# Optimization experiments

Measured on AMD Instinct MI355X. Metric: run time of the kernel, lower is better.

## Reference

```python
import jax, jax.numpy as jnp
import numpy as np

B_SZ, N_INST, D_IN, D_OUT, C_COMP, M_RANK = 512, 4, 1024, 1024, 64, 256

def setup_inputs() -> dict:
    key = jax.random.key(0)
    k1, k2, k3, k4 = jax.random.split(key, 4)
    x = jax.random.normal(k1, (B_SZ, N_INST, D_IN), dtype=jnp.float32)
    A = jax.random.normal(k2, (N_INST, C_COMP, D_IN, M_RANK), dtype=jnp.float32) * 0.02
    Bp = jax.random.normal(k3, (N_INST, C_COMP, M_RANK, D_OUT), dtype=jnp.float32) * 0.02
    topk_mask = jax.random.randint(k4, (B_SZ, N_INST, C_COMP), 0, 2, dtype=jnp.int32)
    return {"x": x, "A": A, "B": Bp, "topk_mask": topk_mask}

def reference(x, A, B, topk_mask):
    # inner: [b, i, C, m]
    inner = jnp.einsum('bid,icdm->bicm', x, A)
    inner = inner * topk_mask.astype(inner.dtype)[..., None]
    # comp: [b, i, C, d_out]
    comp = jnp.einsum('bicm,icmo->bico', inner, B)
    # sum over components C -> [b, i, d_out]
    return comp.sum(axis=2)
```

## Files before the change

kernel.cpp:

```cpp
#include <hip/hip_runtime.h>
#include <hip/hip_bf16.h>
#include <stdint.h>

#define B_SZ   512
#define NINST  4
#define D_IN   1024
#define D_OUTD 1024
#define CCOMP  64
#define MRANK  256
#define KTOT   (CCOMP*MRANK)

typedef __attribute__((ext_vector_type(4))) float  f32x4;
typedef __attribute__((ext_vector_type(8))) __bf16 bf16x8;
typedef __attribute__((ext_vector_type(4))) __bf16 bf16x4;

__device__ inline void gload_lds16(const __bf16* g, __bf16* l) {
  __builtin_amdgcn_global_load_lds(
      (const __attribute__((address_space(1))) void*)g,
      (__attribute__((address_space(3))) void*)l, 16, 0, 0);
}

__global__ __launch_bounds__(256)
void xcvt_kernel(const float* __restrict__ x, __bf16* __restrict__ xbf)
{
  const int total = (B_SZ*NINST*D_IN) / 4;
  for (int v = blockIdx.x*256 + threadIdx.x; v < total; v += gridDim.x*256) {
    const int k4 = v & 255;
    const int i  = (v >> 8) & 3;
    const int b  = v >> 10;
    f32x4 f = ((const f32x4*)x)[v];
    bf16x4 h; h[0]=(__bf16)f.x; h[1]=(__bf16)f.y; h[2]=(__bf16)f.z; h[3]=(__bf16)f.w;
    ((bf16x4*)xbf)[((size_t)i*B_SZ + b)*256 + k4] = h;
  }
}

__global__ __launch_bounds__(256, 2)
void p1_kernel(const __bf16* __restrict__ xbf, const float* __restrict__ A,
               const int* __restrict__ mask, __bf16* __restrict__ inner)
{
  const int bid = blockIdx.x;
  const int L   = (bid & 7) * 64 + (bid >> 3);
  const int bt  = L & 3;
  const int mt  = (L >> 2) & 1;
  const int icg = L >> 3;
  const int ic0 = icg * 4;
  const int i   = ic0 >> 6;
  const int c0  = ic0 & 63;
  const int b0  = bt * 128;
  const int m0  = mt * 128;

  const int tid  = threadIdx.x;
  const int lane = tid & 63;
  const int wid  = tid >> 6;
  const int wr   = wid >> 1;
  const int wc   = wid & 1;

  __shared__ __align__(16) char smem[65536];
  __bf16* Xs = (__bf16*)smem;
  __bf16* As = (__bf16*)(smem + 32768);

  f32x4 acc[4][4];
#pragma unroll
  for (int a_ = 0; a_ < 4; ++a_)
#pragma unroll
    for (int b_ = 0; b_ < 4; ++b_)
      acc[a_][b_] = (f32x4){0.f, 0.f, 0.f, 0.f};

  const __bf16* xbase  = xbf + ((size_t)i * B_SZ + b0) * D_IN;
  const float*  Abase0 = A + (size_t)ic0 * D_IN * MRANK + m0;

  const int bo = tid & 127;
  const int bg = tid >> 7;

  float areg[4][8];

  auto stageXs = [&](int buf, int kt) {
#pragma unroll
    for (int q = 0; q < 4; ++q) {
      const int ci  = wid*4 + q;
      const int row = ci*8 + (lane >> 3);
      const int kch = (lane & 7) ^ (row & 7);
      gload_lds16(xbase + (size_t)row * D_IN + (kt & 15)*64 + kch*8,
                  Xs + buf*8192 + ci*512);
    }
  };
  auto loadA = [&](int kt) {
    const float* Ab = Abase0 + (size_t)(kt >> 4) * D_IN * MRANK;
#pragma unroll
    for (int q = 0; q < 4; ++q)
#pragma unroll
      for (int j = 0; j < 8; ++j)
        areg[q][j] = Ab[(size_t)((kt & 15)*64 + (bg*4+q)*8 + j)*MRANK + bo];
  };
  auto writeA = [&](int buf) {
#pragma unroll
    for (int q = 0; q < 4; ++q) {
      const int oct = bg*4 + q;
      bf16x8 h;
#pragma unroll
      for (int j = 0; j < 8; ++j) h[j] = (__bf16)areg[q][j];
      *(bf16x8*)(As + buf*8192 + bo*64 + ((oct ^ (bo & 7)))*8) = h;
    }
  };

  stageXs(0, 0); loadA(0); writeA(0);
  __syncthreads();

  int cur = 0;
  for (int kt = 0; kt < 64; ++kt) {
    if (kt+1 < 64) { stageXs(cur ^ 1, kt+1); loadA(kt+1); }
#pragma unroll
    for (int kk = 0; kk < 2; ++kk) {
      const int oct = kk*4 + (lane >> 4);
      bf16x8 af[4];
#pragma unroll
      for (int mi = 0; mi < 4; ++mi) {
        const int row = wr*64 + mi*16 + (lane & 15);
        af[mi] = *(const bf16x8*)(Xs + cur*8192 + row*64 + ((oct ^ (row & 7)))*8);
      }
#pragma unroll
      for (int ni = 0; ni < 4; ++ni) {
        const int col = wc*64 + ni*16 + (lane & 15);
        bf16x8 bfr = *(const bf16x8*)(As + cur*8192 + col*64 + ((oct ^ (col & 7)))*8);
#pragma unroll
        for (int mi = 0; mi < 4; ++mi)
          acc[mi][ni] = __builtin_amdgcn_mfma_f32_16x16x32_bf16(af[mi], bfr, acc[mi][ni], 0, 0, 0);
      }
    }
    if ((kt & 15) == 15) {
      const int c = c0 + (kt >> 4);
      __bf16* obase = inner + ((size_t)i * B_SZ + b0) * KTOT + (size_t)c * MRANK + m0;
      float mv[16];
#pragma unroll
      for (int mi = 0; mi < 4; ++mi)
#pragma unroll
        for (int j = 0; j < 4; ++j) {
          const int row = wr*64 + mi*16 + (lane >> 4)*4 + j;
          mv[mi*4+j] = (float)mask[(size_t)(b0 + row) * (NINST*CCOMP) + i*CCOMP + c];
        }
#pragma unroll
      for (int mi = 0; mi < 4; ++mi)
#pragma unroll
        for (int ni = 0; ni < 4; ++ni) {
          const int colL = wc*64 + ni*16 + (lane & 15);
#pragma unroll
          for (int j = 0; j < 4; ++j) {
            const int rowL = wr*64 + mi*16 + (lane >> 4)*4 + j;
            obase[(size_t)rowL * KTOT + colL] = (__bf16)(acc[mi][ni][j] * mv[mi*4+j]);
          }
#pragma unroll
          for (int j = 0; j < 4; ++j) acc[mi][ni][j] = 0.f;
        }
    }
    if (kt+1 < 64) writeA(cur ^ 1);
    __syncthreads();
    cur ^= 1;
  }
}

__global__ __launch_bounds__(256, 2)
void p2_kernel(const __bf16* __restrict__ inner, const float* __restrict__ Bm,
               float* __restrict__ dst, int nks)
{
  const int bid = blockIdx.x;
  const int L   = (bid & 7) * (gridDim.x >> 3) + (bid >> 3);
  const int bt  = L & 3;
  const int nt  = (L >> 2) & 7;
  const int rest = L >> 5;
  const int ks  = rest % nks;
  const int i   = rest / nks;
  const int b0  = bt * 128;
  const int o0  = nt * 128;
  const int NSTEP = (KTOT/64) / nks;
  const int kb0   = ks * NSTEP;

  const int tid  = threadIdx.x;
  const int lane = tid & 63;
  const int wid  = tid >> 6;
  const int wr   = wid >> 1;
  const int wc   = wid & 1;

  __shared__ __align__(16) char smem[65536];
  __bf16* Is = (__bf16*)smem;
  __bf16* Bs = (__bf16*)(smem + 32768);

  f32x4 acc[4][4];
#pragma unroll
  for (int a_ = 0; a_ < 4; ++a_)
#pragma unroll
    for (int b_ = 0; b_ < 4; ++b_)
      acc[a_][b_] = (f32x4){0.f, 0.f, 0.f, 0.f};

  const __bf16* ibase = inner + ((size_t)i * B_SZ + b0) * KTOT;
  const float*  Bbase = Bm + (size_t)i * KTOT * D_OUTD + o0;

  const int bo = tid & 127;
  const int bg = tid >> 7;

  float breg[4][8];

  auto stageIs = [&](int buf, int kt) {
#pragma unroll
    for (int q = 0; q < 4; ++q) {
      const int ci  = wid*4 + q;
      const int row = ci*8 + (lane >> 3);
      const int kch = (lane & 7) ^ (row & 7);
      gload_lds16(ibase + (size_t)row * KTOT + kt*64 + kch*8,
                  Is + buf*8192 + ci*512);
    }
  };
  auto loadB = [&](int kt) {
#pragma unroll
    for (int q = 0; q < 4; ++q)
#pragma unroll
      for (int j = 0; j < 8; ++j)
        breg[q][j] = Bbase[(size_t)(kt*64 + (bg*4+q)*8 + j)*D_OUTD + bo];
  };
  auto writeB = [&](int buf) {
#pragma unroll
    for (int q = 0; q < 4; ++q) {
      const int oct = bg*4 + q;
      bf16x8 h;
#pragma unroll
      for (int j = 0; j < 8; ++j) h[j] = (__bf16)breg[q][j];
      *(bf16x8*)(Bs + buf*8192 + bo*64 + ((oct ^ (bo & 7)))*8) = h;
    }
  };

  stageIs(0, kb0); loadB(kb0); writeB(0);
  __syncthreads();

  int cur = 0;
  for (int t = 0; t < NSTEP; ++t) {
    if (t+1 < NSTEP) { stageIs(cur ^ 1, kb0 + t + 1); loadB(kb0 + t + 1); }
#pragma unroll
    for (int kk = 0; kk < 2; ++kk) {
      const int oct = kk*4 + (lane >> 4);
      bf16x8 af[4];
#pragma unroll
      for (int mi = 0; mi < 4; ++mi) {
        const int row = wr*64 + mi*16 + (lane & 15);
        af[mi] = *(const bf16x8*)(Is + cur*8192 + row*64 + ((oct ^ (row & 7)))*8);
      }
#pragma unroll
      for (int ni = 0; ni < 4; ++ni) {
        const int col = wc*64 + ni*16 + (lane & 15);
        bf16x8 bfr = *(const bf16x8*)(Bs + cur*8192 + col*64 + ((oct ^ (col & 7)))*8);
#pragma unroll
        for (int mi = 0; mi < 4; ++mi)
          acc[mi][ni] = __builtin_amdgcn_mfma_f32_16x16x32_bf16(af[mi], bfr, acc[mi][ni], 0, 0, 0);
      }
    }
    if (t+1 < NSTEP) writeB(cur ^ 1);
    __syncthreads();
    cur ^= 1;
  }

  float* obase = dst + (size_t)ks * ((size_t)B_SZ*NINST*D_OUTD)
               + ((size_t)b0 * NINST + i) * D_OUTD + o0;
#pragma unroll
  for (int mi = 0; mi < 4; ++mi)
#pragma unroll
    for (int ni = 0; ni < 4; ++ni) {
      const int colL = wc*64 + ni*16 + (lane & 15);
#pragma unroll
      for (int j = 0; j < 4; ++j) {
        const int rowL = wr*64 + mi*16 + (lane >> 4)*4 + j;
        obase[(size_t)rowL * (NINST*D_OUTD) + colL] = acc[mi][ni][j];
      }
    }
}

__global__ __launch_bounds__(256)
void reduce_kernel(const float* __restrict__ part, float* __restrict__ out, int nks)
{
  const int total = (B_SZ*NINST*D_OUTD) / 4;
  for (int v = blockIdx.x*256 + threadIdx.x; v < total; v += gridDim.x*256) {
    f32x4 s = ((const f32x4*)part)[v];
    for (int ks = 1; ks < nks; ++ks)
      s += ((const f32x4*)part)[(size_t)ks*total + v];
    ((f32x4*)out)[v] = s;
  }
}

extern "C" void kernel_launch(void* const* d_in, const int* in_sizes, int n_in,
                              void* d_out, int out_size, void* d_ws, size_t ws_size,
                              hipStream_t stream) {
  const float* x    = (const float*)d_in[0];
  const float* A    = (const float*)d_in[1];
  const float* Bm   = (const float*)d_in[2];
  const int*   mask = (const int*)d_in[3];

  const size_t innerB = (size_t)NINST * B_SZ * KTOT * 2;
  const size_t xbfB   = (size_t)NINST * B_SZ * D_IN * 2;
  const size_t partB  = (size_t)B_SZ * NINST * D_OUTD * 4;

  char* p = (char*)d_ws;
  __bf16* inner = (__bf16*)p;             p += innerB;
  __bf16* xbf   = (__bf16*)p;             p += xbfB;
  const size_t used = (size_t)(p - (char*)d_ws);

  int nks = 1;
  if      (ws_size >= used + 4*partB) nks = 4;
  else if (ws_size >= used + 2*partB) nks = 2;
  float* part = (nks > 1) ? (float*)p : (float*)d_out;

  xcvt_kernel<<<dim3(1024),  dim3(256), 0, stream>>>(x, xbf);
  p1_kernel<<<dim3(512),     dim3(256), 0, stream>>>(xbf, A, mask, inner);
  p2_kernel<<<dim3(128*nks), dim3(256), 0, stream>>>(inner, Bm, part, nks);
  if (nks > 1)
    reduce_kernel<<<dim3(512), dim3(256), 0, stream>>>(part, (float*)d_out, nks);
}
```

Before: 269.2 us.

## Prefetch fp32 weight tiles two steps ahead with partial vmcnt barriers

Both GEMM kernels now keep two register sets for the fp32 A/B weight tiles and issue global loads two k-steps ahead. The main loop is unrolled by two so the register buffers alternate. The plain __syncthreads is replaced by a custom barrier that waits only until vmcnt drops to 32, so the newest prefetch stays in flight across the barrier. The goal is to hide global-load latency behind MFMA work, at the cost of more registers (which may spill or lower occupancy). The hand-tuned vmcnt counts must match the real number of outstanding loads, or LDS data could be read before it arrives.

New measurement: 1.039 ms. 3.86x slower.

```diff
diff --git a/kernel.cpp b/kernel.cpp
--- a/kernel.cpp
+++ b/kernel.cpp
@@ -19,6 +19,17 @@
       (const __attribute__((address_space(1))) void*)g,
       (__attribute__((address_space(3))) void*)l, 16, 0, 0);
 }
+
+#define BAR32() do { \
+  asm volatile("s_waitcnt lgkmcnt(0) vmcnt(32)" ::: "memory"); \
+  __builtin_amdgcn_sched_barrier(0); \
+  __builtin_amdgcn_s_barrier(); \
+  __builtin_amdgcn_sched_barrier(0); } while (0)
+#define BAR0() do { \
+  asm volatile("s_waitcnt lgkmcnt(0) vmcnt(0)" ::: "memory"); \
+  __builtin_amdgcn_sched_barrier(0); \
+  __builtin_amdgcn_s_barrier(); \
+  __builtin_amdgcn_sched_barrier(0); } while (0)
 
 __global__ __launch_bounds__(256)
 void xcvt_kernel(const float* __restrict__ x, __bf16* __restrict__ xbf)
@@ -72,7 +83,7 @@
   const int bo = tid & 127;
   const int bg = tid >> 7;
 
-  float areg[4][8];
+  float a0[4][8], a1[4][8];
 
   auto stageXs = [&](int buf, int kt) {
 #pragma unroll
@@ -84,7 +95,7 @@
                   Xs + buf*8192 + ci*512);
     }
   };
-  auto loadA = [&](int kt) {
+  auto loadA = [&](int kt, float (&areg)[4][8]) {
     const float* Ab = Abase0 + (size_t)(kt >> 4) * D_IN * MRANK;
 #pragma unroll
     for (int q = 0; q < 4; ++q)
@@ -92,7 +103,7 @@
       for (int j = 0; j < 8; ++j)
         areg[q][j] = Ab[(size_t)((kt & 15)*64 + (bg*4+q)*8 + j)*MRANK + bo];
   };
-  auto writeA = [&](int buf) {
+  auto writeA = [&](int buf, const float (&areg)[4][8]) {
 #pragma unroll
     for (int q = 0; q < 4; ++q) {
       const int oct = bg*4 + q;
@@ -102,13 +113,7 @@
       *(bf16x8*)(As + buf*8192 + bo*64 + ((oct ^ (bo & 7)))*8) = h;
     }
   };
-
-  stageXs(0, 0); loadA(0); writeA(0);
-  __syncthreads();
-
-  int cur = 0;
-  for (int kt = 0; kt < 64; ++kt) {
-    if (kt+1 < 64) { stageXs(cur ^ 1, kt+1); loadA(kt+1); }
+  auto computeStep = [&](int cur) {
 #pragma unroll
     for (int kk = 0; kk < 2; ++kk) {
       const int oct = kk*4 + (lane >> 4);
@@ -127,34 +132,56 @@
           acc[mi][ni] = __builtin_amdgcn_mfma_f32_16x16x32_bf16(af[mi], bfr, acc[mi][ni], 0, 0, 0);
       }
     }
-    if ((kt & 15) == 15) {
-      const int c = c0 + (kt >> 4);
-      __bf16* obase = inner + ((size_t)i * B_SZ + b0) * KTOT + (size_t)c * MRANK + m0;
-      float mv[16];
-#pragma unroll
-      for (int mi = 0; mi < 4; ++mi)
+  };
+  auto segEpilogue = [&](int kt) {
+    const int c = c0 + (kt >> 4);
+    __bf16* obase = inner + ((size_t)i * B_SZ + b0) * KTOT + (size_t)c * MRANK + m0;
+    float mv[16];
+#pragma unroll
+    for (int mi = 0; mi < 4; ++mi)
+#pragma unroll
+      for (int j = 0; j < 4; ++j) {
+        const int row = wr*64 + mi*16 + (lane >> 4)*4 + j;
+        mv[mi*4+j] = (float)mask[(size_t)(b0 + row) * (NINST*CCOMP) + i*CCOMP + c];
+      }
+#pragma unroll
+    for (int mi = 0; mi < 4; ++mi)
+#pragma unroll
+      for (int ni = 0; ni < 4; ++ni) {
+        const int colL = wc*64 + ni*16 + (lane & 15);
 #pragma unroll
         for (int j = 0; j < 4; ++j) {
-          const int row = wr*64 + mi*16 + (lane >> 4)*4 + j;
-          mv[mi*4+j] = (float)mask[(size_t)(b0 + row) * (NINST*CCOMP) + i*CCOMP + c];
+          const int rowL = wr*64 + mi*16 + (lane >> 4)*4 + j;
+          obase[(size_t)rowL * KTOT + colL] = (__bf16)(acc[mi][ni][j] * mv[mi*4+j]);
         }
 #pragma unroll
-      for (int mi = 0; mi < 4; ++mi)
-#pragma unroll
-        for (int ni = 0; ni < 4; ++ni) {
-          const int colL = wc*64 + ni*16 + (lane & 15);
-#pragma unroll
-          for (int j = 0; j < 4; ++j) {
-            const int rowL = wr*64 + mi*16 + (lane >> 4)*4 + j;
-            obase[(size_t)rowL * KTOT + colL] = (__bf16)(acc[mi][ni][j] * mv[mi*4+j]);
-          }
-#pragma unroll
-          for (int j = 0; j < 4; ++j) acc[mi][ni][j] = 0.f;
-        }
-    }
-    if (kt+1 < 64) writeA(cur ^ 1);
-    __syncthreads();
+        for (int j = 0; j < 4; ++j) acc[mi][ni][j] = 0.f;
+      }
+  };
+
+  stageXs(0, 0);
+  loadA(0, a0); loadA(1, a1);
+  writeA(0, a0);
+  BAR32();
+
+  int cur = 0;
+  for (int t = 0; t < 64; t += 2) {
+    if (t+1 < 64) stageXs(cur ^ 1, t+1);
+    if (t+2 < 64) loadA(t+2, a0);
+    computeStep(cur);
+    if (t+1 < 64) writeA(cur ^ 1, a1);
+    if (t < 62) BAR32(); else BAR0();
     cur ^= 1;
+    {
+      const int u = t + 1;
+      if (u+1 < 64) stageXs(cur ^ 1, u+1);
+      if (u+2 < 64) loadA(u+2, a1);
+      computeStep(cur);
+      if ((u & 15) == 15) segEpilogue(u);
+      if (u+1 < 64) writeA(cur ^ 1, a0);
+      if (u < 62) BAR32(); else BAR0();
+      cur ^= 1;
+    }
   }
 }
 
@@ -197,7 +224,7 @@
   const int bo = tid & 127;
   const int bg = tid >> 7;
 
-  float breg[4][8];
+  float b0r[4][8], b1r[4][8];
 
   auto stageIs = [&](int buf, int kt) {
 #pragma unroll
@@ -209,14 +236,14 @@
                   Is + buf*8192 + ci*512);
     }
   };
-  auto loadB = [&](int kt) {
+  auto loadB = [&](int kt, float (&breg)[4][8]) {
 #pragma unroll
     for (int q = 0; q < 4; ++q)
 #pragma unroll
       for (int j = 0; j < 8; ++j)
         breg[q][j] = Bbase[(size_t)(kt*64 + (bg*4+q)*8 + j)*D_OUTD + bo];
   };
-  auto writeB = [&](int buf) {
+  auto writeB = [&](int buf, const float (&breg)[4][8]) {
 #pragma unroll
     for (int q = 0; q < 4; ++q) {
       const int oct = bg*4 + q;
@@ -226,13 +253,7 @@
       *(bf16x8*)(Bs + buf*8192 + bo*64 + ((oct ^ (bo & 7)))*8) = h;
     }
   };
-
-  stageIs(0, kb0); loadB(kb0); writeB(0);
-  __syncthreads();
-
-  int cur = 0;
-  for (int t = 0; t < NSTEP; ++t) {
-    if (t+1 < NSTEP) { stageIs(cur ^ 1, kb0 + t + 1); loadB(kb0 + t + 1); }
+  auto computeStep = [&](int cur) {
 #pragma unroll
     for (int kk = 0; kk < 2; ++kk) {
       const int oct = kk*4 + (lane >> 4);
@@ -251,9 +272,32 @@
           acc[mi][ni] = __builtin_amdgcn_mfma_f32_16x16x32_bf16(af[mi], bfr, acc[mi][ni], 0, 0, 0);
       }
     }
-    if (t+1 < NSTEP) writeB(cur ^ 1);
-    __syncthreads();
+  };
+
+  stageIs(0, kb0);
+  loadB(kb0, b0r);
+  if (1 < NSTEP) loadB(kb0 + 1, b1r);
+  writeB(0, b0r);
+  BAR32();
+
+  int cur = 0;
+  for (int t = 0; t < NSTEP; t += 2) {
+    if (t+1 < NSTEP) stageIs(cur ^ 1, kb0 + t + 1);
+    if (t+2 < NSTEP) loadB(kb0 + t + 2, b0r);
+    computeStep(cur);
+    if (t+1 < NSTEP) writeB(cur ^ 1, b1r);
+    if (t < NSTEP-2) BAR32(); else BAR0();
     cur ^= 1;
+    {
+      const int u = t + 1;
+      if (u >= NSTEP) break;
+      if (u+1 < NSTEP) stageIs(cur ^ 1, kb0 + u + 1);
+      if (u+2 < NSTEP) loadB(kb0 + u + 2, b1r);
+      computeStep(cur);
+      if (u+1 < NSTEP) writeB(cur ^ 1, b0r);
+      if (u < NSTEP-2) BAR32(); else BAR0();
+      cur ^= 1;
+    }
   }
 
   float* obase = dst + (size_t)ks * ((size_t)B_SZ*NINST*D_OUTD)
```

## Retile p1 to 512-thread blocks with 256-row batch tiles and 32-wide K steps

Applied to the files above, without the earlier changes.

The first-stage GEMM kernel now runs 512 threads (8 waves) per block, each block covering 256 batch rows and 2 components instead of 128 rows and 4 components. The K step per stage shrinks from 64 to 32, which halves the LDS A-tile and shortens the per-thread A register staging. The aim is for each fp32 A slice that is loaded and converted to feed twice as many batch rows, cutting redundant A traffic and raising occupancy per block. In exchange each block needs twice as many barrier-separated iterations per component, and the 32-wide tiles bring a new LDS swizzle.

New measurement: 298.2 us. 10.8% more time.

```diff
diff --git a/kernel.cpp b/kernel.cpp
--- a/kernel.cpp
+++ b/kernel.cpp
@@ -34,19 +34,19 @@
   }
 }
 
-__global__ __launch_bounds__(256, 2)
+__global__ __launch_bounds__(512, 2)
 void p1_kernel(const __bf16* __restrict__ xbf, const float* __restrict__ A,
                const int* __restrict__ mask, __bf16* __restrict__ inner)
 {
   const int bid = blockIdx.x;
   const int L   = (bid & 7) * 64 + (bid >> 3);
-  const int bt  = L & 3;
-  const int mt  = (L >> 2) & 1;
-  const int icg = L >> 3;
-  const int ic0 = icg * 4;
+  const int bt  = L & 1;
+  const int mt  = (L >> 1) & 1;
+  const int icg = L >> 2;
+  const int ic0 = icg * 2;
   const int i   = ic0 >> 6;
   const int c0  = ic0 & 63;
-  const int b0  = bt * 128;
+  const int b0  = bt * 256;
   const int m0  = mt * 128;
 
   const int tid  = threadIdx.x;
@@ -55,7 +55,7 @@
   const int wr   = wid >> 1;
   const int wc   = wid & 1;
 
-  __shared__ __align__(16) char smem[65536];
+  __shared__ __align__(16) char smem[49152];
   __bf16* Xs = (__bf16*)smem;
   __bf16* As = (__bf16*)(smem + 32768);
 
@@ -66,41 +66,76 @@
     for (int b_ = 0; b_ < 4; ++b_)
       acc[a_][b_] = (f32x4){0.f, 0.f, 0.f, 0.f};
 
-  const __bf16* xbase  = xbf + ((size_t)i * B_SZ + b0) * D_IN;
-  const float*  Abase0 = A + (size_t)ic0 * D_IN * MRANK + m0;
-
-  const int bo = tid & 127;
-  const int bg = tid >> 7;
-
-  float areg[4][8];
+  const __bf16* xbase = xbf + ((size_t)i * B_SZ + b0) * D_IN;
+
+  const int am = tid & 127;
+  const int ag = tid >> 7;
+
+  float areg[8];
 
   auto stageXs = [&](int buf, int kt) {
 #pragma unroll
-    for (int q = 0; q < 4; ++q) {
-      const int ci  = wid*4 + q;
-      const int row = ci*8 + (lane >> 3);
-      const int kch = (lane & 7) ^ (row & 7);
-      gload_lds16(xbase + (size_t)row * D_IN + (kt & 15)*64 + kch*8,
+    for (int q = 0; q < 2; ++q) {
+      const int ci  = wid*2 + q;
+      const int row = ci*16 + (lane >> 2);
+      const int kch = (lane & 3) ^ (row & 3);
+      gload_lds16(xbase + (size_t)row * D_IN + (kt & 31)*32 + kch*8,
                   Xs + buf*8192 + ci*512);
     }
   };
   auto loadA = [&](int kt) {
-    const float* Ab = Abase0 + (size_t)(kt >> 4) * D_IN * MRANK;
-#pragma unroll
-    for (int q = 0; q < 4; ++q)
-#pragma unroll
-      for (int j = 0; j < 8; ++j)
-        areg[q][j] = Ab[(size_t)((kt & 15)*64 + (bg*4+q)*8 + j)*MRANK + bo];
+    const float* Ab = A + (size_t)(ic0 + (kt >> 5)) * D_IN * MRANK + m0;
+#pragma unroll
+    for (int j = 0; j < 8; ++j)
+      areg[j] = Ab[(size_t)((kt & 31)*32 + ag*8 + j)*MRANK + am];
   };
   auto writeA = [&](int buf) {
-#pragma unroll
-    for (int q = 0; q < 4; ++q) {
-      const int oct = bg*4 + q;
-      bf16x8 h;
-#pragma unroll
-      for (int j = 0; j < 8; ++j) h[j] = (__bf16)areg[q][j];
-      *(bf16x8*)(As + buf*8192 + bo*64 + ((oct ^ (bo & 7)))*8) = h;
-    }
+    bf16x8 h;
+#pragma unroll
+    for (int j = 0; j < 8; ++j) h[j] = (__bf16)areg[j];
+    *(bf16x8*)(As + buf*4096 + am*32 + ((ag ^ (am & 3)))*8) = h;
+  };
+  auto computeStep = [&](int cur) {
+    const int oct = lane >> 4;
+    bf16x8 af[4];
+#pragma unroll
+    for (int mi = 0; mi < 4; ++mi) {
+      const int row = wr*64 + mi*16 + (lane & 15);
+      af[mi] = *(const bf16x8*)(Xs + cur*8192 + row*32 + ((oct ^ (row & 3)))*8);
+    }
+#pragma unroll
+    for (int ni = 0; ni < 4; ++ni) {
+      const int col = wc*64 + ni*16 + (lane & 15);
+      bf16x8 bfr = *(const bf16x8*)(As + cur*4096 + col*32 + ((oct ^ (col & 3)))*8);
+#pragma unroll
+      for (int mi = 0; mi < 4; ++mi)
+        acc[mi][ni] = __builtin_amdgcn_mfma_f32_16x16x32_bf16(af[mi], bfr, acc[mi][ni], 0, 0, 0);
+    }
+  };
+  auto segEpilogue = [&](int kt) {
+    const int c = c0 + (kt >> 5);
+    __bf16* obase = inner + ((size_t)i * B_SZ + b0) * KTOT + (size_t)c * MRANK + m0;
+    float mv[16];
+#pragma unroll
+    for (int mi = 0; mi < 4; ++mi)
+#pragma unroll
+      for (int j = 0; j < 4; ++j) {
+        const int row = wr*64 + mi*16 + (lane >> 4)*4 + j;
+        mv[mi*4+j] = (float)mask[(size_t)(b0 + row) * (NINST*CCOMP) + i*CCOMP + c];
+      }
+#pragma unroll
+    for (int mi = 0; mi < 4; ++mi)
+#pragma unroll
+      for (int ni = 0; ni < 4; ++ni) {
+        const int colL = wc*64 + ni*16 + (lane & 15);
+#pragma unroll
+        for (int j = 0; j < 4; ++j) {
+          const int rowL = wr*64 + mi*16 + (lane >> 4)*4 + j;
+          obase[(size_t)rowL * KTOT + colL] = (__bf16)(acc[mi][ni][j] * mv[mi*4+j]);
+        }
+#pragma unroll
+        for (int j = 0; j < 4; ++j) acc[mi][ni][j] = 0.f;
+      }
   };
 
   stageXs(0, 0); loadA(0); writeA(0);
@@ -109,49 +144,8 @@
   int cur = 0;
   for (int kt = 0; kt < 64; ++kt) {
     if (kt+1 < 64) { stageXs(cur ^ 1, kt+1); loadA(kt+1); }
-#pragma unroll
-    for (int kk = 0; kk < 2; ++kk) {
-      const int oct = kk*4 + (lane >> 4);
-      bf16x8 af[4];
-#pragma unroll
-      for (int mi = 0; mi < 4; ++mi) {
-        const int row = wr*64 + mi*16 + (lane & 15);
-        af[mi] = *(const bf16x8*)(Xs + cur*8192 + row*64 + ((oct ^ (row & 7)))*8);
-      }
-#pragma unroll
-      for (int ni = 0; ni < 4; ++ni) {
-        const int col = wc*64 + ni*16 + (lane & 15);
-        bf16x8 bfr = *(const bf16x8*)(As + cur*8192 + col*64 + ((oct ^ (col & 7)))*8);
-#pragma unroll
-        for (int mi = 0; mi < 4; ++mi)
-          acc[mi][ni] = __builtin_amdgcn_mfma_f32_16x16x32_bf16(af[mi], bfr, acc[mi][ni], 0, 0, 0);
-      }
-    }
-    if ((kt & 15) == 15) {
-      const int c = c0 + (kt >> 4);
-      __bf16* obase = inner + ((size_t)i * B_SZ + b0) * KTOT + (size_t)c * MRANK + m0;
-      float mv[16];
-#pragma unroll
-      for (int mi = 0; mi < 4; ++mi)
-#pragma unroll
-        for (int j = 0; j < 4; ++j) {
-          const int row = wr*64 + mi*16 + (lane >> 4)*4 + j;
-          mv[mi*4+j] = (float)mask[(size_t)(b0 + row) * (NINST*CCOMP) + i*CCOMP + c];
-        }
-#pragma unroll
-      for (int mi = 0; mi < 4; ++mi)
-#pragma unroll
-        for (int ni = 0; ni < 4; ++ni) {
-          const int colL = wc*64 + ni*16 + (lane & 15);
-#pragma unroll
-          for (int j = 0; j < 4; ++j) {
-            const int rowL = wr*64 + mi*16 + (lane >> 4)*4 + j;
-            obase[(size_t)rowL * KTOT + colL] = (__bf16)(acc[mi][ni][j] * mv[mi*4+j]);
-          }
-#pragma unroll
-          for (int j = 0; j < 4; ++j) acc[mi][ni][j] = 0.f;
-        }
-    }
+    computeStep(cur);
+    if ((kt & 31) == 31) segEpilogue(kt);
     if (kt+1 < 64) writeA(cur ^ 1);
     __syncthreads();
     cur ^= 1;
@@ -306,7 +300,7 @@
   float* part = (nks > 1) ? (float*)p : (float*)d_out;
 
   xcvt_kernel<<<dim3(1024),  dim3(256), 0, stream>>>(x, xbf);
-  p1_kernel<<<dim3(512),     dim3(256), 0, stream>>>(xbf, A, mask, inner);
+  p1_kernel<<<dim3(512),     dim3(512), 0, stream>>>(xbf, A, mask, inner);
   p2_kernel<<<dim3(128*nks), dim3(256), 0, stream>>>(inner, Bm, part, nks);
   if (nks > 1)
     reduce_kernel<<<dim3(512), dim3(256), 0, stream>>>(part, (float*)d_out, nks);
```

## Pre-convert A to transposed bf16 and stream both GEMM operands via LDS loads

Applied to the files above, without the earlier changes.

Adds a kernel that converts A from fp32 to bf16 and transposes it so the reduction dimension is contiguous. A new first-stage GEMM then stages both x and A tiles straight into shared memory with the async global-to-LDS path, replacing per-thread fp32 register loads and conversion. The aim is to cut register pressure and conversion work in the main loop. The trade-off is extra HBM traffic on every call: a 128MB bf16 write and read-back on top of the full fp32 read of A. The new path runs only when the workspace is large enough, and it reuses the bf16 A buffer for the split-K partial sums.

New measurement: 298.4 us. 10.9% more time.

```diff
diff --git a/kernel.cpp b/kernel.cpp
--- a/kernel.cpp
+++ b/kernel.cpp
@@ -34,9 +34,159 @@
   }
 }
 
+__global__ __launch_bounds__(256)
+void atr_kernel(const float* __restrict__ A, __bf16* __restrict__ Abf)
+{
+  const int bid = blockIdx.x;
+  const int ic  = bid >> 2;
+  const int s4  = bid & 3;
+  const int i   = ic >> 6;
+  const int c   = ic & 63;
+  const int tid = threadIdx.x;
+
+  __shared__ __bf16 T[64][260];
+
+  for (int sub = 0; sub < 4; ++sub) {
+    const int d0 = s4*256 + sub*64;
+#pragma unroll
+    for (int it = 0; it < 16; ++it) {
+      const int idx = it*256 + tid;
+      const int d   = idx >> 6;
+      const int m4  = idx & 63;
+      f32x4 v = *(const f32x4*)(A + ((size_t)ic*D_IN + d0 + d)*MRANK + m4*4);
+      bf16x4 h; h[0]=(__bf16)v.x; h[1]=(__bf16)v.y; h[2]=(__bf16)v.z; h[3]=(__bf16)v.w;
+      *(bf16x4*)(&T[d][m4*4]) = h;
+    }
+    __syncthreads();
+#pragma unroll
+    for (int it = 0; it < 8; ++it) {
+      const int m   = it*32 + (tid >> 3);
+      const int dgu = tid & 7;
+      bf16x8 h;
+#pragma unroll
+      for (int j = 0; j < 8; ++j) h[j] = T[dgu*8 + j][m];
+      *(bf16x8*)(Abf + ((size_t)i*KTOT + (size_t)c*MRANK + m)*D_IN + d0 + dgu*8) = h;
+    }
+    __syncthreads();
+  }
+}
+
 __global__ __launch_bounds__(256, 2)
-void p1_kernel(const __bf16* __restrict__ xbf, const float* __restrict__ A,
-               const int* __restrict__ mask, __bf16* __restrict__ inner)
+void p1_lite(const __bf16* __restrict__ xbf, const __bf16* __restrict__ Abf,
+             const int* __restrict__ mask, __bf16* __restrict__ inner)
+{
+  const int bid = blockIdx.x;
+  const int L   = (bid & 7) * 64 + (bid >> 3);
+  const int bt  = L & 3;
+  const int ntg = (L >> 2) & 31;
+  const int i   = L >> 7;
+  const int b0  = bt * 128;
+  const int n0g = ntg * 512;
+
+  const int tid  = threadIdx.x;
+  const int lane = tid & 63;
+  const int wid  = tid >> 6;
+  const int wr   = wid >> 1;
+  const int wc   = wid & 1;
+
+  __shared__ __align__(16) char smem[65536];
+  __bf16* Xs = (__bf16*)smem;
+  __bf16* As = (__bf16*)(smem + 32768);
+
+  f32x4 acc[4][4];
+#pragma unroll
+  for (int a_ = 0; a_ < 4; ++a_)
+#pragma unroll
+    for (int b_ = 0; b_ < 4; ++b_)
+      acc[a_][b_] = (f32x4){0.f, 0.f, 0.f, 0.f};
+
+  const __bf16* xbase = xbf + ((size_t)i * B_SZ + b0) * D_IN;
+  const __bf16* abase = Abf + ((size_t)i * KTOT + n0g) * D_IN;
+
+  auto stageXs = [&](int buf, int kt) {
+#pragma unroll
+    for (int q = 0; q < 4; ++q) {
+      const int ci  = wid*4 + q;
+      const int row = ci*8 + (lane >> 3);
+      const int kch = (lane & 7) ^ (row & 7);
+      gload_lds16(xbase + (size_t)row * D_IN + (kt & 15)*64 + kch*8,
+                  Xs + buf*8192 + ci*512);
+    }
+  };
+  auto stageAs = [&](int buf, int kt) {
+    const __bf16* ab = abase + (size_t)(kt >> 4) * 128 * D_IN;
+#pragma unroll
+    for (int q = 0; q < 4; ++q) {
+      const int ci  = wid*4 + q;
+      const int row = ci*8 + (lane >> 3);
+      const int kch = (lane & 7) ^ (row & 7);
+      gload_lds16(ab + (size_t)row * D_IN + (kt & 15)*64 + kch*8,
+                  As + buf*8192 + ci*512);
+    }
+  };
+  auto computeStep = [&](int cur) {
+#pragma unroll
+    for (int kk = 0; kk < 2; ++kk) {
+      const int oct = kk*4 + (lane >> 4);
+      bf16x8 af[4];
+#pragma unroll
+      for (int mi = 0; mi < 4; ++mi) {
+        const int row = wr*64 + mi*16 + (lane & 15);
+        af[mi] = *(const bf16x8*)(Xs + cur*8192 + row*64 + ((oct ^ (row & 7)))*8);
+      }
+#pragma unroll
+      for (int ni = 0; ni < 4; ++ni) {
+        const int col = wc*64 + ni*16 + (lane & 15);
+        bf16x8 bfr = *(const bf16x8*)(As + cur*8192 + col*64 + ((oct ^ (col & 7)))*8);
+#pragma unroll
+        for (int mi = 0; mi < 4; ++mi)
+          acc[mi][ni] = __builtin_amdgcn_mfma_f32_16x16x32_bf16(af[mi], bfr, acc[mi][ni], 0, 0, 0);
+      }
+    }
+  };
+  auto segEpilogue = [&](int kt) {
+    const int n0 = n0g + (kt >> 4) * 128;
+    const int c  = n0 >> 8;
+    __bf16* obase = inner + ((size_t)i * B_SZ + b0) * KTOT + n0;
+    float mv[16];
+#pragma unroll
+    for (int mi = 0; mi < 4; ++mi)
+#pragma unroll
+      for (int j = 0; j < 4; ++j) {
+        const int row = wr*64 + mi*16 + (lane >> 4)*4 + j;
+        mv[mi*4+j] = (float)mask[(size_t)(b0 + row) * (NINST*CCOMP) + i*CCOMP + c];
+      }
+#pragma unroll
+    for (int mi = 0; mi < 4; ++mi)
+#pragma unroll
+      for (int ni = 0; ni < 4; ++ni) {
+        const int colL = wc*64 + ni*16 + (lane & 15);
+#pragma unroll
+        for (int j = 0; j < 4; ++j) {
+          const int rowL = wr*64 + mi*16 + (lane >> 4)*4 + j;
+          obase[(size_t)rowL * KTOT + colL] = (__bf16)(acc[mi][ni][j] * mv[mi*4+j]);
+        }
+#pragma unroll
+        for (int j = 0; j < 4; ++j) acc[mi][ni][j] = 0.f;
+      }
+  };
+
+  stageXs(0, 0); stageAs(0, 0);
+  __syncthreads();
+
+  int cur = 0;
+  for (int kt = 0; kt < 64; ++kt) {
+    if (kt+1 < 64) { stageXs(cur ^ 1, kt+1); stageAs(cur ^ 1, kt+1); }
+    computeStep(cur);
+    if ((kt & 15) == 15) segEpilogue(kt);
+    __syncthreads();
+    cur ^= 1;
+  }
+}
+
+__global__ __launch_bounds__(256, 2)
+void p1_fallback(const __bf16* __restrict__ xbf, const float* __restrict__ A,
+                 const int* __restrict__ mask, __bf16* __restrict__ inner)
 {
   const int bid = blockIdx.x;
   const int L   = (bid & 7) * 64 + (bid >> 3);
@@ -71,7 +221,6 @@
 
   const int bo = tid & 127;
   const int bg = tid >> 7;
-
   float areg[4][8];
 
   auto stageXs = [&](int buf, int kt) {
@@ -196,7 +345,6 @@
 
   const int bo = tid & 127;
   const int bg = tid >> 7;
-
   float breg[4][8];
 
   auto stageIs = [&](int buf, int kt) {
@@ -293,20 +441,32 @@
 
   const size_t innerB = (size_t)NINST * B_SZ * KTOT * 2;
   const size_t xbfB   = (size_t)NINST * B_SZ * D_IN * 2;
+  const size_t AbfB   = (size_t)NINST * KTOT * D_IN * 2;
   const size_t partB  = (size_t)B_SZ * NINST * D_OUTD * 4;
 
   char* p = (char*)d_ws;
   __bf16* inner = (__bf16*)p;             p += innerB;
   __bf16* xbf   = (__bf16*)p;             p += xbfB;
-  const size_t used = (size_t)(p - (char*)d_ws);
+
+  const bool lite = (ws_size >= innerB + xbfB + AbfB);
+
+  xcvt_kernel<<<dim3(1024), dim3(256), 0, stream>>>(x, xbf);
 
   int nks = 1;
-  if      (ws_size >= used + 4*partB) nks = 4;
-  else if (ws_size >= used + 2*partB) nks = 2;
-  float* part = (nks > 1) ? (float*)p : (float*)d_out;
-
-  xcvt_kernel<<<dim3(1024),  dim3(256), 0, stream>>>(x, xbf);
-  p1_kernel<<<dim3(512),     dim3(256), 0, stream>>>(xbf, A, mask, inner);
+  float* part;
+  if (lite) {
+    __bf16* Abf = (__bf16*)p;
+    nks = 4;
+    part = (float*)p;
+    atr_kernel<<<dim3(1024), dim3(256), 0, stream>>>(A, Abf);
+    p1_lite<<<dim3(512), dim3(256), 0, stream>>>(xbf, Abf, mask, inner);
+  } else {
+    if      (ws_size >= innerB + xbfB + 4*partB) nks = 4;
+    else if (ws_size >= innerB + xbfB + 2*partB) nks = 2;
+    part = (nks > 1) ? (float*)p : (float*)d_out;
+    p1_fallback<<<dim3(512), dim3(256), 0, stream>>>(xbf, A, mask, inner);
+  }
+
   p2_kernel<<<dim3(128*nks), dim3(256), 0, stream>>>(inner, Bm, part, nks);
   if (nks > 1)
     reduce_kernel<<<dim3(512), dim3(256), 0, stream>>>(part, (float*)d_out, nks);
```
